# Optimization experiments

Hardware: AMD Instinct MI355X
Metric: run time of the kernel (lower is better)

Reference implementation:

```python
import jax, jax.numpy as jnp
import numpy as np

D = 1024      # d_model
H = 16        # nhead
DH = D // H   # d_head = 64
DC = D // 4   # d_compress = 256
HID = 2048    # dim_feedforward (SwiGLU hidden)
G = 2         # num_groups
EPG = 4       # experts_per_gp
E = G * EPG   # num_experts = 8
TOPK = 2
EPS = 1e-6
B, T = 2, 2048


def _rope_sincos(t, dh):
    inv_freq = 1.0 / (10000.0 ** (jnp.arange(0, dh, 2, dtype=jnp.float32) / dh))
    ang = jnp.arange(t, dtype=jnp.float32)[:, None] * inv_freq[None, :]  # [T, dh/2]
    return jnp.sin(ang), jnp.cos(ang)


def _apply_rope(x, sin, cos):
    # x: [B, H, T, DH]; sin/cos: [T, DH/2] broadcast over B,H
    x1 = x[..., ::2]
    x2 = x[..., 1::2]
    r = jnp.stack([x1 * cos - x2 * sin, x1 * sin + x2 * cos], axis=-1)
    return r.reshape(x.shape)


def _swiglu(x):
    a, b = jnp.split(x, 2, axis=-1)
    return jax.nn.silu(a) * b


def _rmsnorm(x, w):
    return x * jax.lax.rsqrt(jnp.mean(x * x, axis=-1, keepdims=True) + EPS) * w


def reference(src, Wq, Wk_c, Wv_c, Wk, Wv, Wo,
              W_shared_in, W_shared_out, W1_shared, W2_experts,
              Wg_gate, We_gate, group_bias, expert_bias, norm1_w, norm2_w):
    Bb, Tt, C = src.shape
    # ---- Latent attention (K/V compressed to d_c then re-expanded) ----
    q = (src @ Wq).reshape(Bb, Tt, H, DH).transpose(0, 2, 1, 3)
    k = ((src @ Wk_c) @ Wk).reshape(Bb, Tt, H, DH).transpose(0, 2, 1, 3)
    v = ((src @ Wv_c) @ Wv).reshape(Bb, Tt, H, DH).transpose(0, 2, 1, 3)
    sin, cos = _rope_sincos(Tt, DH)
    q = _apply_rope(q, sin, cos)
    k = _apply_rope(k, sin, cos)
    attn = jnp.einsum('bhqd,bhkd->bhqk', q, k) / np.sqrt(DH).astype(np.float32)
    attn = jax.nn.softmax(attn, axis=-1)
    sa = jnp.einsum('bhqk,bhkd->bhqd', attn, v)
    sa = sa.transpose(0, 2, 1, 3).reshape(Bb, Tt, C) @ Wo
    x = _rmsnorm(src + sa, norm1_w)

    # ---- Hierarchical MoE FFN ----
    S = Bb * Tt
    flat = x.reshape(S, C)
    shared = _swiglu(flat @ W_shared_in) @ W_shared_out          # [S, C]
    g_probs = jax.nn.softmax(flat @ Wg_gate + group_bias, -1)    # [S, G]
    g_idx = jnp.argmax(g_probs, axis=-1)                          # [S]
    e_logits = flat @ We_gate + expert_bias                       # [S, E]
    e_group = jnp.arange(E) // EPG
    in_group = e_group[None, :] == g_idx[:, None]                 # [S, E]
    e_probs = jax.nn.softmax(jnp.where(in_group, e_logits, -jnp.inf), -1)
    g_prob = jnp.take_along_axis(g_probs, g_idx[:, None], axis=1)  # [S, 1]
    p_expert = e_probs * g_prob
    topv, topi = jax.lax.top_k(p_expert, TOPK)                    # [S, K]
    # dense combine weights: zero for non-selected experts (same math as dispatch loop)
    w = jnp.zeros((S, E), flat.dtype).at[jnp.arange(S)[:, None], topi].set(topv)
    h = _swiglu(flat @ W1_shared)                                 # [S, HID] (w1 shared by all experts)
    routed = jnp.zeros_like(shared)
    for e in range(E):  # fixed small expert count
        routed = routed + (h @ W2_experts[e]) * w[:, e:e + 1]
    out = x + (shared + routed).reshape(Bb, Tt, C)
    return _rmsnorm(out, norm2_w)


def setup_inputs() -> dict:
    key = jax.random.key(0)
    ks = jax.random.split(key, 14)
    s = 0.02
    return {
        'src': jax.random.normal(ks[0], (B, T, D), jnp.float32),
        'Wq': jax.random.normal(ks[1], (D, D), jnp.float32) * s,
        'Wk_c': jax.random.normal(ks[2], (D, DC), jnp.float32) * s,
        'Wv_c': jax.random.normal(ks[3], (D, DC), jnp.float32) * s,
        'Wk': jax.random.normal(ks[4], (DC, D), jnp.float32) * s,
        'Wv': jax.random.normal(ks[5], (DC, D), jnp.float32) * s,
        'Wo': jax.random.normal(ks[6], (D, D), jnp.float32) * s,
        'W_shared_in': jax.random.normal(ks[7], (D, 2 * HID), jnp.float32) * s,
        'W_shared_out': jax.random.normal(ks[8], (HID, D), jnp.float32) * s,
        'W1_shared': jax.random.normal(ks[9], (D, 2 * HID), jnp.float32) * s,
        'W2_experts': jax.random.normal(ks[10], (E, HID, D), jnp.float32) * s,
        'Wg_gate': jax.random.normal(ks[11], (D, G), jnp.float32) * s,
        'We_gate': jax.random.normal(ks[12], (D, E), jnp.float32) * s,
        'group_bias': jnp.zeros((G,), jnp.float32),
        'expert_bias': jnp.zeros((E,), jnp.float32),
        'norm1_w': jnp.ones((D,), jnp.float32),
        'norm2_w': jnp.ones((D,), jnp.float32),
    }
```

## Files before the change

kernel.cpp:

```cpp
#include <hip/hip_runtime.h>
#include <math.h>

#define D_    1024
#define H_    16
#define DH_   64
#define DC_   256
#define HID_  2048
#define E_    8
#define B_    2
#define T_    2048
#define S_    4096
#define EPS_  1e-6f
#define QKVW_ 3072

typedef unsigned short u16;
typedef short bf16x8 __attribute__((ext_vector_type(8)));
typedef float f32x4 __attribute__((ext_vector_type(4)));

__device__ __forceinline__ float b2f(u16 u) {
    return __uint_as_float(((unsigned int)u) << 16);
}
__device__ __forceinline__ u16 f2b(float f) {
    unsigned int u = __float_as_uint(f);
    u += 0x7FFF + ((u >> 16) & 1);
    return (u16)(u >> 16);
}
__device__ __forceinline__ void g2l16(const u16* g, u16* l) {
    __builtin_amdgcn_global_load_lds(
        (const __attribute__((address_space(1))) void*)g,
        (__attribute__((address_space(3))) void*)l, 16, 0, 0);
}

__global__ __launch_bounds__(256) void conv_t(const float* __restrict__ in,
                                              u16* __restrict__ out,
                                              int K, int N,
                                              long inZ, long outZ, int perm) {
    in  += (long)blockIdx.z * inZ;
    out += (long)blockIdx.z * outZ;
    __shared__ float t[32][33];
    const int n0 = blockIdx.x * 32, k0 = blockIdx.y * 32;
    int src_n0 = n0;
    if (perm) {
        int t64 = n0 >> 6;
        src_n0 = ((n0 & 63) == 0) ? t64 * 32 : (N / 2 + t64 * 32);
    }
    const int tx = threadIdx.x & 31, ty = threadIdx.x >> 5;
#pragma unroll
    for (int i = 0; i < 4; i++)
        t[ty + 8 * i][tx] = in[(long)(k0 + ty + 8 * i) * N + src_n0 + tx];
    __syncthreads();
#pragma unroll
    for (int i = 0; i < 4; i++)
        out[(long)(n0 + ty + 8 * i) * K + k0 + tx] = f2b(t[tx][ty + 8 * i]);
}

__global__ __launch_bounds__(256) void vt_conv(const u16* __restrict__ qkv,
                                               u16* __restrict__ vt) {
    __shared__ u16 t[32][34];
    const int bh = blockIdx.z;
    const int b = bh >> 4, h = bh & 15;
    const int t0 = blockIdx.x * 32, d0 = blockIdx.y * 32;
    const int tx = threadIdx.x & 31, ty = threadIdx.x >> 5;
#pragma unroll
    for (int i = 0; i < 4; i++)
        t[ty + 8 * i][tx] =
            qkv[((long)b * T_ + t0 + ty + 8 * i) * QKVW_ + 2048 + h * 64 + d0 + tx];
    __syncthreads();
#pragma unroll
    for (int i = 0; i < 4; i++)
        vt[((long)bh * 64 + d0 + ty + 8 * i) * T_ + t0 + tx] = t[tx][ty + 8 * i];
}

__global__ __launch_bounds__(256) void convert_bf16(const float* __restrict__ in,
                                                    u16* __restrict__ out, int n4) {
    int i = blockIdx.x * 256 + threadIdx.x;
    if (i >= n4) return;
    float4 f = ((const float4*)in)[i];
    ushort4 o;
    o.x = f2b(f.x); o.y = f2b(f.y); o.z = f2b(f.z); o.w = f2b(f.w);
    ((ushort4*)out)[i] = o;
}

template<int OUTMODE>
__global__ __launch_bounds__(256) void gemm_bf16(const u16* __restrict__ A,
                                                 const u16* __restrict__ Bt,
                                                 void* __restrict__ Cp,
                                                 int N, int K, int ldo,
                                                 void* __restrict__ Cp2) {
    __shared__ u16 As[128 * 32];
    __shared__ u16 Bs[128 * 32];
    const int tid  = threadIdx.x;
    const int lane = tid & 63;
    const int wv   = tid >> 6;
    const int wm   = wv >> 1, wn = wv & 1;
    const long row0 = (long)blockIdx.y * 128;
    const long col0 = (long)blockIdx.x * 128;
    const int Klocal = K / gridDim.z;
    const long koff  = (long)blockIdx.z * Klocal;

    f32x4 acc[4][4];
#pragma unroll
    for (int i = 0; i < 4; i++)
#pragma unroll
        for (int j = 0; j < 4; j++) acc[i][j] = (f32x4){0.f, 0.f, 0.f, 0.f};

    const int sr = tid >> 2;
    const int sc = (tid & 3) << 3;
    const u16* Ag  = A  + (row0 + sr) * (long)K + koff + sc;
    const u16* Ag2 = Ag + 64 * (long)K;
    const u16* Bg  = Bt + (col0 + sr) * (long)K + koff + sc;
    const u16* Bg2 = Bg + 64 * (long)K;
    u16* lA  = As + tid * 8;
    u16* lA2 = As + 2048 + tid * 8;
    u16* lB  = Bs + tid * 8;
    u16* lB2 = Bs + 2048 + tid * 8;

    const int fl = lane & 15;
    const int fk = (lane >> 4) << 3;
    const u16* ArA = As + (wm * 64 + fl) * 32 + fk;
    const u16* BrB = Bs + (wn * 64 + fl) * 32 + fk;

    for (int k0 = 0; k0 < Klocal; k0 += 32) {
        __syncthreads();
        g2l16(Ag + k0, lA);
        g2l16(Ag2 + k0, lA2);
        g2l16(Bg + k0, lB);
        g2l16(Bg2 + k0, lB2);
        __syncthreads();
        bf16x8 af[4], bfr[4];
#pragma unroll
        for (int mi = 0; mi < 4; mi++) af[mi]  = *(const bf16x8*)(ArA + mi * 512);
#pragma unroll
        for (int ni = 0; ni < 4; ni++) bfr[ni] = *(const bf16x8*)(BrB + ni * 512);
#pragma unroll
        for (int mi = 0; mi < 4; mi++)
#pragma unroll
            for (int ni = 0; ni < 4; ni++)
                acc[mi][ni] = __builtin_amdgcn_mfma_f32_16x16x32_bf16(
                    af[mi], bfr[ni], acc[mi][ni], 0, 0, 0);
    }

    const int cr = (lane >> 4) << 2;
    const int cc = lane & 15;
#pragma unroll
    for (int mi = 0; mi < 4; mi++) {
#pragma unroll
        for (int r = 0; r < 4; r++) {
            long grow = row0 + wm * 64 + mi * 16 + cr + r;
#pragma unroll
            for (int ni = 0; ni < 4; ni++) {
                long gcol = col0 + wn * 64 + ni * 16 + cc;
                float v = acc[mi][ni][r];
                if (OUTMODE == 1)      ((u16*)Cp)[grow * ldo + gcol] = f2b(v);
                else if (OUTMODE == 2) ((u16*)Cp)[gcol * ldo + grow] = f2b(v);
                else {
                    float* basep = (float*)(blockIdx.z ? Cp2 : Cp);
                    basep[grow * ldo + gcol] = v;
                }
            }
        }
    }
}

template<int OUTMODE>
__global__ __launch_bounds__(512) void gemm256(const u16* __restrict__ A,
                                               const u16* __restrict__ Bt,
                                               void* __restrict__ Cp,
                                               int K, int ldo) {
    __shared__ u16 As[2][256 * 64];
    __shared__ u16 Bs[2][256 * 64];
    const int tid  = threadIdx.x;
    const int lane = tid & 63;
    const int w    = tid >> 6;
    const int wr   = w >> 2, wc = w & 3;
    const long row0 = (long)blockIdx.y * 256;
    const long col0 = (long)blockIdx.x * 256;

    f32x4 acc[8][4];
#pragma unroll
    for (int i = 0; i < 8; i++)
#pragma unroll
        for (int j = 0; j < 4; j++) acc[i][j] = (f32x4){0.f, 0.f, 0.f, 0.f};

    const int srow = tid >> 3;
    const int sgS  = ((tid & 7) ^ (srow & 7)) << 3;
    const u16* Ag = A  + (row0 + srow) * (long)K + sgS;
    const u16* Bg = Bt + (col0 + srow) * (long)K + sgS;

    const int fl = lane & 15;
    const int fq = lane >> 4;
    const int aoff = (wr * 128 + fl) * 64;
    const int boff = (wc * 64 + fl) * 64;

#define STAGE256(j, buf) do {                                             \
        const long ko_ = (long)(j) * 64;                                  \
        u16* la_ = As[buf] + tid * 8;                                     \
        u16* lb_ = Bs[buf] + tid * 8;                                     \
        _Pragma("unroll")                                                 \
        for (int rr_ = 0; rr_ < 4; rr_++)                                 \
            g2l16(Ag + (long)rr_ * 64 * K + ko_, la_ + rr_ * 4096);       \
        _Pragma("unroll")                                                 \
        for (int rr_ = 0; rr_ < 4; rr_++)                                 \
            g2l16(Bg + (long)rr_ * 64 * K + ko_, lb_ + rr_ * 4096);       \
    } while (0)

    STAGE256(0, 0);
    __syncthreads();
    const int NT = K >> 6;
    for (int j = 0; j < NT; j++) {
        const int buf = j & 1;
        if (j + 1 < NT) STAGE256(j + 1, buf ^ 1);
        const u16* ab = As[buf];
        const u16* bb = Bs[buf];
#pragma unroll
        for (int ks = 0; ks < 2; ks++) {
            const int sw = ((ks * 4 + fq) ^ (fl & 7)) << 3;
            bf16x8 af[8], bfr[4];
#pragma unroll
            for (int mi = 0; mi < 8; mi++)
                af[mi] = *(const bf16x8*)(ab + aoff + mi * 1024 + sw);
#pragma unroll
            for (int ni = 0; ni < 4; ni++)
                bfr[ni] = *(const bf16x8*)(bb + boff + ni * 1024 + sw);
#pragma unroll
            for (int mi = 0; mi < 8; mi++)
#pragma unroll
                for (int ni = 0; ni < 4; ni++)
                    acc[mi][ni] = __builtin_amdgcn_mfma_f32_16x16x32_bf16(
                        af[mi], bfr[ni], acc[mi][ni], 0, 0, 0);
        }
        __syncthreads();
    }

    const int cr = fq << 2;
    const int cc = fl;
#pragma unroll
    for (int mi = 0; mi < 8; mi++) {
#pragma unroll
        for (int r = 0; r < 4; r++) {
            long grow = row0 + wr * 128 + mi * 16 + cr + r;
            if (OUTMODE == 3) {
                u16* outb = (u16*)Cp + (long)(blockIdx.x >> 4) * S_ * HID_;
                u16* hrow = outb + grow * ldo + (blockIdx.x & 15) * 128 + wc * 32;
#pragma unroll
                for (int ni = 0; ni < 2; ni++) {
                    float a = acc[mi][ni][r], b = acc[mi][ni + 2][r];
                    float sig = 1.f / (1.f + __expf(-a));
                    hrow[ni * 16 + cc] = f2b(a * sig * b);
                }
            } else {
#pragma unroll
                for (int ni = 0; ni < 4; ni++) {
                    long gcol = col0 + wc * 64 + ni * 16 + cc;
                    ((u16*)Cp)[grow * ldo + gcol] = f2b(acc[mi][ni][r]);
                }
            }
        }
    }
#undef STAGE256
}

__global__ __launch_bounds__(256) void gemm128p(const u16* __restrict__ A,
                                                const u16* __restrict__ Bt,
                                                float* __restrict__ Cp,
                                                int K, int ldo,
                                                float* __restrict__ Cp2) {
    __shared__ u16 As[2][128 * 64];
    __shared__ u16 Bs[2][128 * 64];
    const int tid  = threadIdx.x;
    const int lane = tid & 63;
    const int wv   = tid >> 6;
    const int wm   = wv >> 1, wn = wv & 1;
    const long row0 = (long)blockIdx.y * 128;
    const long col0 = (long)blockIdx.x * 128;
    const int Klocal = K / gridDim.z;
    const long koff  = (long)blockIdx.z * Klocal;

    f32x4 acc[4][4];
#pragma unroll
    for (int i = 0; i < 4; i++)
#pragma unroll
        for (int j = 0; j < 4; j++) acc[i][j] = (f32x4){0.f, 0.f, 0.f, 0.f};

    const int srow = tid >> 3;
    const int sgS  = ((tid & 7) ^ (srow & 7)) << 3;
    const u16* Ag = A  + (row0 + srow) * (long)K + koff + sgS;
    const u16* Bg = Bt + (col0 + srow) * (long)K + koff + sgS;

    const int fl = lane & 15;
    const int fq = lane >> 4;
    const int aoff = (wm * 64 + fl) * 64;
    const int boff = (wn * 64 + fl) * 64;

#define STAGE128(j, buf) do {                                             \
        const long ko_ = (long)(j) * 64;                                  \
        u16* la_ = As[buf] + tid * 8;                                     \
        u16* lb_ = Bs[buf] + tid * 8;                                     \
        _Pragma("unroll")                                                 \
        for (int rr_ = 0; rr_ < 4; rr_++)                                 \
            g2l16(Ag + (long)rr_ * 32 * K + ko_, la_ + rr_ * 2048);       \
        _Pragma("unroll")                                                 \
        for (int rr_ = 0; rr_ < 4; rr_++)                                 \
            g2l16(Bg + (long)rr_ * 32 * K + ko_, lb_ + rr_ * 2048);       \
    } while (0)

    STAGE128(0, 0);
    __syncthreads();
    const int NT = Klocal >> 6;
    for (int j = 0; j < NT; j++) {
        const int buf = j & 1;
        if (j + 1 < NT) STAGE128(j + 1, buf ^ 1);
        const u16* ab = As[buf];
        const u16* bb = Bs[buf];
#pragma unroll
        for (int ks = 0; ks < 2; ks++) {
            const int sw = ((ks * 4 + fq) ^ (fl & 7)) << 3;
            bf16x8 af[4], bfr[4];
#pragma unroll
            for (int mi = 0; mi < 4; mi++)
                af[mi] = *(const bf16x8*)(ab + aoff + mi * 1024 + sw);
#pragma unroll
            for (int ni = 0; ni < 4; ni++)
                bfr[ni] = *(const bf16x8*)(bb + boff + ni * 1024 + sw);
#pragma unroll
            for (int mi = 0; mi < 4; mi++)
#pragma unroll
                for (int ni = 0; ni < 4; ni++)
                    acc[mi][ni] = __builtin_amdgcn_mfma_f32_16x16x32_bf16(
                        af[mi], bfr[ni], acc[mi][ni], 0, 0, 0);
        }
        __syncthreads();
    }

    float* basep = blockIdx.z ? Cp2 : Cp;
    const int cr = fq << 2;
#pragma unroll
    for (int mi = 0; mi < 4; mi++) {
#pragma unroll
        for (int r = 0; r < 4; r++) {
            long grow = row0 + wm * 64 + mi * 16 + cr + r;
#pragma unroll
            for (int ni = 0; ni < 4; ni++) {
                long gcol = col0 + wn * 64 + ni * 16 + fl;
                basep[grow * ldo + gcol] = acc[mi][ni][r];
            }
        }
    }
#undef STAGE128
}

__global__ __launch_bounds__(256) void routed_gemm(const u16* __restrict__ Hh,
                                                   const u16* __restrict__ W2T,
                                                   const int* __restrict__ list,
                                                   const float* __restrict__ wlist,
                                                   const int* __restrict__ bases,
                                                   const int* __restrict__ counts,
                                                   float* __restrict__ Cout) {
    const int e    = blockIdx.y >> 5;
    const int tile = blockIdx.y & 31;
    const int cnt  = counts[e];
    if (tile * 128 >= cnt) return;
    const int base = bases[e];

    __shared__ u16 As[2][128 * 64];
    __shared__ u16 Bs[2][128 * 64];
    __shared__ int   toks[128];
    __shared__ float wrow[128];

    const int tid = threadIdx.x;
    if (tid < 128) {
        int ridx = tile * 128 + tid;
        if (ridx < cnt) { toks[tid] = list[base + ridx]; wrow[tid] = wlist[base + ridx]; }
        else            { toks[tid] = -1;                wrow[tid] = 0.f; }
    }
    __syncthreads();

    const int lane = tid & 63;
    const int wv   = tid >> 6;
    const int wm   = wv >> 1, wn = wv & 1;
    const long col0 = (long)blockIdx.x * 128;

    f32x4 acc[4][4];
#pragma unroll
    for (int i = 0; i < 4; i++)
#pragma unroll
        for (int j = 0; j < 4; j++) acc[i][j] = (f32x4){0.f, 0.f, 0.f, 0.f};

    const int srow = tid >> 3;
    const int sgS  = ((tid & 7) ^ (srow & 7)) << 3;
    const u16* Apt[4];
#pragma unroll
    for (int rr = 0; rr < 4; rr++) {
        int t = toks[srow + 32 * rr];
        Apt[rr] = Hh + (long)(t < 0 ? 0 : t) * HID_ + sgS;
    }
    const u16* Bg = W2T + (long)e * D_ * HID_ + (col0 + srow) * (long)HID_ + sgS;

    const int fl = lane & 15;
    const int fq = lane >> 4;
    const int aoff = (wm * 64 + fl) * 64;
    const int boff = (wn * 64 + fl) * 64;

#define STAGER(j, buf) do {                                               \
        const long ko_ = (long)(j) * 64;                                  \
        u16* la_ = As[buf] + tid * 8;                                     \
        u16* lb_ = Bs[buf] + tid * 8;                                     \
        _Pragma("unroll")                                                 \
        for (int rr_ = 0; rr_ < 4; rr_++)                                 \
            g2l16(Apt[rr_] + ko_, la_ + rr_ * 2048);                      \
        _Pragma("unroll")                                                 \
        for (int rr_ = 0; rr_ < 4; rr_++)                                 \
            g2l16(Bg + (long)rr_ * 32 * HID_ + ko_, lb_ + rr_ * 2048);    \
    } while (0)

    STAGER(0, 0);
    __syncthreads();
    const int NT = HID_ >> 6;
    for (int j = 0; j < NT; j++) {
        const int buf = j & 1;
        if (j + 1 < NT) STAGER(j + 1, buf ^ 1);
        const u16* ab = As[buf];
        const u16* bb = Bs[buf];
#pragma unroll
        for (int ks = 0; ks < 2; ks++) {
            const int sw = ((ks * 4 + fq) ^ (fl & 7)) << 3;
            bf16x8 af[4], bfr[4];
#pragma unroll
            for (int mi = 0; mi < 4; mi++)
                af[mi] = *(const bf16x8*)(ab + aoff + mi * 1024 + sw);
#pragma unroll
            for (int ni = 0; ni < 4; ni++)
                bfr[ni] = *(const bf16x8*)(bb + boff + ni * 1024 + sw);
#pragma unroll
            for (int mi = 0; mi < 4; mi++)
#pragma unroll
                for (int ni = 0; ni < 4; ni++)
                    acc[mi][ni] = __builtin_amdgcn_mfma_f32_16x16x32_bf16(
                        af[mi], bfr[ni], acc[mi][ni], 0, 0, 0);
        }
        __syncthreads();
    }

    const int cr = fq << 2;
    const int cc = fl;
#pragma unroll
    for (int mi = 0; mi < 4; mi++) {
#pragma unroll
        for (int r = 0; r < 4; r++) {
            int rr = wm * 64 + mi * 16 + cr + r;
            int tk = toks[rr];
            if (tk < 0) continue;
            float wvw = wrow[rr];
            float* crow = Cout + (long)tk * D_ + col0 + wn * 64;
#pragma unroll
            for (int ni = 0; ni < 4; ni++)
                atomicAdd(crow + ni * 16 + cc, acc[mi][ni][r] * wvw);
        }
    }
#undef STAGER
}

__global__ __launch_bounds__(256) void rope_table(float2* __restrict__ tab) {
    int idx = blockIdx.x * 256 + threadIdx.x;
    int t = idx >> 5, i = idx & 31;
    float ang = (float)t * powf(10000.f, -(float)i / 32.f);
    float sn, cs;
    sincosf(ang, &sn, &cs);
    tab[idx] = make_float2(sn, cs);
}

__global__ __launch_bounds__(256) void rope_apply(u16* __restrict__ qkv,
                                                  const float2* __restrict__ tab) {
    long p = (long)blockIdx.x * 256 + threadIdx.x;
    int s  = (int)(p >> 8);
    int c8 = (int)(p & 255) << 3;
    int t  = s & (T_ - 1);
    const float2* tp = tab + t * 32 + ((c8 & 63) >> 1);
    u16* px = qkv + (long)s * QKVW_ + c8;
    bf16x8 v = *(const bf16x8*)px;
    bf16x8 o;
#pragma unroll
    for (int j = 0; j < 4; j++) {
        float x1 = b2f((u16)v[2 * j]), x2 = b2f((u16)v[2 * j + 1]);
        float2 sc = tp[j];
        o[2 * j]     = (short)f2b(x1 * sc.y - x2 * sc.x);
        o[2 * j + 1] = (short)f2b(x1 * sc.x + x2 * sc.y);
    }
    *(bf16x8*)px = o;
}

__global__ __launch_bounds__(512) void attn_kernel(const u16* __restrict__ qkv,
                                                   const u16* __restrict__ vtg,
                                                   u16* __restrict__ sab) {
    __shared__ u16 Ks[128 * 64];
    __shared__ u16 Vs[64 * 128];
    __shared__ u16 Ps[8][16 * 128];
    const int tid  = threadIdx.x;
    const int lane = tid & 63;
    const int w    = tid >> 6;
    const int flat = blockIdx.x + (blockIdx.y << 4);
    const int virt = ((flat & 7) << 6) | (flat >> 3);
    const int qt = virt & 15;
    const int bh = virt >> 4;
    const int b  = bh >> 4, h = bh & 15;
    const long tok0 = (long)b * T_ + qt * 128;
    const int fl = lane & 15;
    const int fq = lane >> 4;

    bf16x8 qf0, qf1;
    {
        const u16* qp = qkv + (tok0 + w * 16 + fl) * QKVW_ + h * 64 + fq * 8;
        qf0 = *(const bf16x8*)qp;
        qf1 = *(const bf16x8*)(qp + 32);
    }

    const u16* kb0 = qkv + ((long)b * T_) * QKVW_ + 1024 + h * 64;
    const u16* vb0 = vtg + ((long)bh * 64) * T_;

    const int kr0 = tid >> 3,         kgg = tid & 7;
    const int kr1 = (tid + 512) >> 3;
    const int vr0 = tid >> 4,         vgg = tid & 15;
    const int vr1 = (tid + 512) >> 4;
    const u16* kp0 = kb0 + (long)kr0 * QKVW_ + ((kgg ^ (kr0 & 7)) << 3);
    const u16* kp1 = kb0 + (long)kr1 * QKVW_ + ((kgg ^ (kr1 & 7)) << 3);
    const u16* vp0 = vb0 + (long)vr0 * T_ + ((vgg ^ (vr0 & 15)) << 3);
    const u16* vp1 = vb0 + (long)vr1 * T_ + ((vgg ^ (vr1 & 15)) << 3);
    u16* kl0 = Ks + tid * 8;
    u16* kl1 = Ks + (tid + 512) * 8;
    u16* vl0 = Vs + tid * 8;
    u16* vl1 = Vs + (tid + 512) * 8;

    bf16x8 kreg0, kreg1, vreg0, vreg1;
    auto stage_load = [&](int kt) {
        const long ko = (long)kt * 128 * QKVW_;
        const int  vo = kt * 128;
        kreg0 = *(const bf16x8*)(kp0 + ko);
        kreg1 = *(const bf16x8*)(kp1 + ko);
        vreg0 = *(const bf16x8*)(vp0 + vo);
        vreg1 = *(const bf16x8*)(vp1 + vo);
    };
    auto stage_write = [&]() {
        *(bf16x8*)kl0 = kreg0;
        *(bf16x8*)kl1 = kreg1;
        *(bf16x8*)vl0 = vreg0;
        *(bf16x8*)vl1 = vreg1;
    };

    float m_[4], l_[4];
    f32x4 oacc[4];
#pragma unroll
    for (int i = 0; i < 4; i++) {
        m_[i] = -1e30f; l_[i] = 0.f;
        oacc[i] = (f32x4){0.f, 0.f, 0.f, 0.f};
    }

    stage_load(0);
    stage_write();
    __syncthreads();

    for (int kt = 0; kt < T_ / 128; kt++) {
        const bool pf = (kt + 1 < T_ / 128);
        if (pf) stage_load(kt + 1);

        f32x4 sacc[8];
#pragma unroll
        for (int ni = 0; ni < 8; ni++) sacc[ni] = (f32x4){0.f, 0.f, 0.f, 0.f};
        __builtin_amdgcn_s_setprio(1);
#pragma unroll
        for (int ks = 0; ks < 2; ks++) {
            bf16x8 qq = ks ? qf1 : qf0;
#pragma unroll
            for (int ni = 0; ni < 8; ni++) {
                bf16x8 kf = *(const bf16x8*)(Ks + (ni * 16 + fl) * 64 +
                                             (((ks * 4 + fq) ^ (fl & 7)) << 3));
                sacc[ni] = __builtin_amdgcn_mfma_f32_16x16x32_bf16(qq, kf, sacc[ni], 0, 0, 0);
            }
        }
        __builtin_amdgcn_s_setprio(0);

        float rmax[4];
#pragma unroll
        for (int r = 0; r < 4; r++) {
            float mm = sacc[0][r];
#pragma unroll
            for (int ni = 1; ni < 8; ni++) mm = fmaxf(mm, sacc[ni][r]);
            rmax[r] = mm * 0.125f;
        }
#pragma unroll
        for (int off = 1; off < 16; off <<= 1)
#pragma unroll
            for (int r = 0; r < 4; r++) rmax[r] = fmaxf(rmax[r], __shfl_xor(rmax[r], off));

        bool grow = false;
        float nm[4];
#pragma unroll
        for (int r = 0; r < 4; r++) {
            nm[r] = fmaxf(m_[r], rmax[r]);
            grow = grow || (rmax[r] > m_[r] + 8.f);
        }
        if (__any(grow)) {
#pragma unroll
            for (int r = 0; r < 4; r++) {
                float a = __expf(m_[r] - nm[r]);
                m_[r] = nm[r];
                l_[r] *= a;
#pragma unroll
                for (int ni = 0; ni < 4; ni++) oacc[ni][r] *= a;
            }
        }

        float psum[4];
#pragma unroll
        for (int r = 0; r < 4; r++) psum[r] = 0.f;
        u16* pst = Ps[w];
#pragma unroll
        for (int ni = 0; ni < 8; ni++) {
            int colg = ni * 2 + (fl >> 3);
            int cl   = fl & 7;
#pragma unroll
            for (int r = 0; r < 4; r++) {
                int row = fq * 4 + r;
                float p = __expf(sacc[ni][r] * 0.125f - m_[r]);
                psum[r] += p;
                pst[row * 128 + ((colg ^ (row & 15)) << 3) + cl] = f2b(p);
            }
        }
#pragma unroll
        for (int off = 1; off < 16; off <<= 1)
#pragma unroll
            for (int r = 0; r < 4; r++) psum[r] += __shfl_xor(psum[r], off);
#pragma unroll
        for (int r = 0; r < 4; r++) l_[r] += psum[r];

        __builtin_amdgcn_s_setprio(1);
#pragma unroll
        for (int ks = 0; ks < 4; ks++) {
            bf16x8 pfr = *(const bf16x8*)(pst + fl * 128 +
                                          (((ks * 4 + fq) ^ fl) << 3));
#pragma unroll
            for (int ni = 0; ni < 4; ni++) {
                bf16x8 vf = *(const bf16x8*)(Vs + (ni * 16 + fl) * 128 +
                                             (((ks * 4 + fq) ^ fl) << 3));
                oacc[ni] = __builtin_amdgcn_mfma_f32_16x16x32_bf16(pfr, vf, oacc[ni], 0, 0, 0);
            }
        }
        __builtin_amdgcn_s_setprio(0);

        __syncthreads();
        if (pf) {
            stage_write();
            __syncthreads();
        }
    }

#pragma unroll
    for (int r = 0; r < 4; r++) {
        float inv = 1.f / l_[r];
        u16* op = sab + (tok0 + w * 16 + fq * 4 + r) * D_ + h * 64 + fl;
#pragma unroll
        for (int ni = 0; ni < 4; ni++) op[ni * 16] = f2b(oacc[ni][r] * inv);
    }
}

template<int BF>
__global__ __launch_bounds__(256) void rmsnorm_res(const float* __restrict__ a,
                                                   const float* __restrict__ b,
                                                   const float* __restrict__ b2,
                                                   const float* __restrict__ w,
                                                   float* __restrict__ outf,
                                                   u16* __restrict__ outb) {
    const int s = blockIdx.x;
    const float* ar = a + (long)s * D_;
    const float* br = b + (long)s * D_;
    const float* cr2 = b2 + (long)s * D_;
    float y[4];
    float ss = 0.f;
#pragma unroll
    for (int kx = 0; kx < 4; kx++) {
        int j = threadIdx.x + kx * 256;
        y[kx] = ar[j] + br[j] + cr2[j];
        ss += y[kx] * y[kx];
    }
    __shared__ float red[4];
#pragma unroll
    for (int off = 32; off > 0; off >>= 1) ss += __shfl_down(ss, off);
    int lane = threadIdx.x & 63, wv = threadIdx.x >> 6;
    if (lane == 0) red[wv] = ss;
    __syncthreads();
    float tot = red[0] + red[1] + red[2] + red[3];
    float scl = rsqrtf(tot / (float)D_ + EPS_);
    float* orow = outf + (long)s * D_;
#pragma unroll
    for (int kx = 0; kx < 4; kx++) {
        int j = threadIdx.x + kx * 256;
        float v = y[kx] * scl * w[j];
        orow[j] = v;
        if (BF) outb[(long)s * D_ + j] = f2b(v);
    }
}

__global__ __launch_bounds__(256) void gate_kernel(const float* __restrict__ x,
                                                   const float* __restrict__ Wg,
                                                   const float* __restrict__ We,
                                                   const float* __restrict__ gb,
                                                   const float* __restrict__ eb,
                                                   int* __restrict__ tok_e,
                                                   float* __restrict__ tok_w) {
    const int wave = threadIdx.x >> 6;
    const int lane = threadIdx.x & 63;
    const int s = blockIdx.x * 4 + wave;
    const float* xr = x + (long)s * D_;
    float g0 = 0.f, g1 = 0.f;
    float ee[8];
#pragma unroll
    for (int e = 0; e < 8; e++) ee[e] = 0.f;
    for (int j = lane; j < D_; j += 64) {
        float xv = xr[j];
        g0 += xv * Wg[j * 2 + 0];
        g1 += xv * Wg[j * 2 + 1];
#pragma unroll
        for (int e = 0; e < 8; e++) ee[e] += xv * We[j * 8 + e];
    }
#pragma unroll
    for (int off = 32; off > 0; off >>= 1) {
        g0 += __shfl_down(g0, off);
        g1 += __shfl_down(g1, off);
#pragma unroll
        for (int e = 0; e < 8; e++) ee[e] += __shfl_down(ee[e], off);
    }
    if (lane == 0) {
        g0 += gb[0];
        g1 += gb[1];
        int gidx = (g1 > g0) ? 1 : 0;
        float gm = fmaxf(g0, g1);
        float p0 = expf(g0 - gm), p1 = expf(g1 - gm);
        float gprob = (gidx ? p1 : p0) / (p0 + p1);
        int base = gidx * 4;
        float pe[4];
        float em = -1e30f;
#pragma unroll
        for (int i = 0; i < 4; i++) {
            pe[i] = ee[base + i] + eb[base + i];
            em = fmaxf(em, pe[i]);
        }
        float sum = 0.f;
#pragma unroll
        for (int i = 0; i < 4; i++) { pe[i] = expf(pe[i] - em); sum += pe[i]; }
        float inv = gprob / sum;
#pragma unroll
        for (int i = 0; i < 4; i++) pe[i] *= inv;
        int i1 = 0;
        for (int i = 1; i < 4; i++) if (pe[i] > pe[i1]) i1 = i;
        int i2 = -1;
        for (int i = 0; i < 4; i++) {
            if (i == i1) continue;
            if (i2 < 0 || pe[i] > pe[i2]) i2 = i;
        }
        tok_e[s * 2 + 0] = base + i1;
        tok_e[s * 2 + 1] = base + i2;
        tok_w[s * 2 + 0] = pe[i1];
        tok_w[s * 2 + 1] = pe[i2];
    }
}

__global__ __launch_bounds__(256) void route_build(const int* __restrict__ tok_e,
                                                   const float* __restrict__ tok_w,
                                                   int* __restrict__ counts_g,
                                                   int* __restrict__ bases_g,
                                                   int* __restrict__ list,
                                                   float* __restrict__ wlist) {
    __shared__ int cnt[E_], bas[E_], cur[E_];
    const int tid = threadIdx.x;
    if (tid < E_) cnt[tid] = 0;
    __syncthreads();
    for (int i = tid; i < 2 * S_; i += 256) atomicAdd(&cnt[tok_e[i]], 1);
    __syncthreads();
    if (tid == 0) {
        int acc = 0;
        for (int e = 0; e < E_; e++) { bas[e] = acc; cur[e] = acc; acc += cnt[e]; }
    }
    __syncthreads();
    if (tid < E_) { counts_g[tid] = cnt[tid]; bases_g[tid] = bas[tid]; }
    for (int i = tid; i < 2 * S_; i += 256) {
        int e = tok_e[i];
        int p = atomicAdd(&cur[e], 1);
        list[p] = i >> 1;
        wlist[p] = tok_w[i];
    }
}

extern "C" void kernel_launch(void* const* d_in, const int* in_sizes, int n_in,
                              void* d_out, int out_size, void* d_ws, size_t ws_size,
                              hipStream_t stream) {
    const float* src  = (const float*)d_in[0];
    const float* Wq   = (const float*)d_in[1];
    const float* Wk_c = (const float*)d_in[2];
    const float* Wv_c = (const float*)d_in[3];
    const float* Wk   = (const float*)d_in[4];
    const float* Wv   = (const float*)d_in[5];
    const float* Wo   = (const float*)d_in[6];
    const float* Wsin = (const float*)d_in[7];
    const float* Wsout= (const float*)d_in[8];
    const float* W1   = (const float*)d_in[9];
    const float* W2   = (const float*)d_in[10];
    const float* Wg   = (const float*)d_in[11];
    const float* We   = (const float*)d_in[12];
    const float* gb   = (const float*)d_in[13];
    const float* eb   = (const float*)d_in[14];
    const float* n1w  = (const float*)d_in[15];
    const float* n2w  = (const float*)d_in[16];
    float* out = (float*)d_out;

    const size_t MB = 1u << 20;
    char* w8 = (char*)d_ws;
    u16*  qkv   = (u16*)(w8);
    u16*  vtg   = (u16*)(w8 + 24 * MB);
    float* oproj0 = (float*)(w8);
    float* oproj1 = (float*)(w8 + 16 * MB);
    u16*  w2t   = (u16*)(w8);
    u16*  WkcB  = (u16*)(w8 + 24 * MB);
    u16*  WvcB  = (u16*)(w8 + 24 * MB + 512 * 1024);
    u16*  WkTs  = (u16*)(w8 + 25 * MB);
    u16*  WvTs  = (u16*)(w8 + 25 * MB + 512 * 1024);
    u16*  sab   = (u16*)(w8 + 32 * MB);
    float* tokw = (float*)(w8 + 32 * MB);
    float* wlist = tokw + 2 * S_;
    int* toke   = (int*)(wlist + 2 * S_);
    int* list   = toke + 2 * S_;
    int* counts = list + 2 * S_;
    int* bases  = counts + E_;
    float* x1   = (float*)(w8 + 40 * MB);
    float* ffn0 = (float*)(w8 + 56 * MB);
    u16*  x1b   = (u16*)(w8 + 72 * MB);
    u16*  hbuf  = (u16*)(w8 + 80 * MB);
    u16*  srcb  = (u16*)(w8 + 96 * MB);
    float2* rtab= (float2*)(w8 + 104 * MB);
    u16*  hbuf2 = (u16*)(w8 + 96 * MB);
    u16*  WqkvT = (u16*)(w8 + 112 * MB);
    u16*  WsoutT= (u16*)(w8 + 112 * MB);
    u16*  WoT   = (u16*)(w8 + 118 * MB);
    u16*  WsinT = (u16*)(w8 + 120 * MB);
    u16*  W1T   = (u16*)(w8 + 128 * MB);
    float* ffn1 = (float*)(w8 + 120 * MB);

    dim3 blk(256);

    conv_t<<<dim3(32, 32), blk, 0, stream>>>(Wq, WqkvT, 1024, 1024, 0, 0, 0);
    convert_bf16<<<dim3(D_ * DC_ / 4 / 256), blk, 0, stream>>>(Wk_c, WkcB, D_ * DC_ / 4);
    convert_bf16<<<dim3(D_ * DC_ / 4 / 256), blk, 0, stream>>>(Wv_c, WvcB, D_ * DC_ / 4);
    conv_t<<<dim3(32, 8), blk, 0, stream>>>(Wk, WkTs, 256, 1024, 0, 0, 0);
    conv_t<<<dim3(32, 8), blk, 0, stream>>>(Wv, WvTs, 256, 1024, 0, 0, 0);
    gemm_bf16<2><<<dim3(8, 8), blk, 0, stream>>>(WkcB, WkTs, WqkvT + 1024 * 1024, 1024, 256, 1024, nullptr);
    gemm_bf16<2><<<dim3(8, 8), blk, 0, stream>>>(WvcB, WvTs, WqkvT + 2048 * 1024, 1024, 256, 1024, nullptr);

    convert_bf16<<<dim3(S_ * D_ / 4 / 256), blk, 0, stream>>>(src, srcb, S_ * D_ / 4);

    gemm256<1><<<dim3(QKVW_ / 256, S_ / 256), dim3(512), 0, stream>>>(srcb, WqkvT, qkv, 1024, QKVW_);

    conv_t<<<dim3(32, 32), blk, 0, stream>>>(Wo, WoT, 1024, 1024, 0, 0, 0);
    conv_t<<<dim3(128, 32), blk, 0, stream>>>(Wsin, WsinT, 1024, 4096, 0, 0, 1);
    conv_t<<<dim3(32, 64), blk, 0, stream>>>(Wsout, WsoutT, 2048, 1024, 0, 0, 0);
    conv_t<<<dim3(128, 32), blk, 0, stream>>>(W1, W1T, 1024, 4096, 0, 0, 1);

    rope_table<<<dim3(T_ * 32 / 256), blk, 0, stream>>>(rtab);
    rope_apply<<<dim3(S_ * 2048 / 8 / 256), blk, 0, stream>>>(qkv, rtab);

    vt_conv<<<dim3(T_ / 32, 2, B_ * H_), blk, 0, stream>>>(qkv, vtg);
    attn_kernel<<<dim3(T_ / 128, B_ * H_), dim3(512), 0, stream>>>(qkv, vtg, sab);

    gemm128p<<<dim3(8, 32, 2), blk, 0, stream>>>(sab, WoT, oproj0, 1024, 1024, oproj1);
    rmsnorm_res<1><<<dim3(S_), blk, 0, stream>>>(src, oproj0, oproj1, n1w, x1, x1b);

    gemm256<3><<<dim3(8192 / 256, S_ / 256), dim3(512), 0, stream>>>(x1b, WsinT, hbuf, 1024, 2048);

    gemm128p<<<dim3(8, 32, 2), blk, 0, stream>>>(hbuf, WsoutT, ffn0, 2048, 1024, ffn1);

    gate_kernel<<<dim3(S_ / 4), blk, 0, stream>>>(x1, Wg, We, gb, eb, toke, tokw);
    route_build<<<dim3(1), blk, 0, stream>>>(toke, tokw, counts, bases, list, wlist);

    conv_t<<<dim3(32, 64, 8), blk, 0, stream>>>(W2, w2t, 2048, 1024,
                                                (long)HID_ * D_, (long)D_ * HID_, 0);
    routed_gemm<<<dim3(8, E_ * 32), blk, 0, stream>>>(hbuf2, w2t, list, wlist,
                                                      bases, counts, ffn0);

    rmsnorm_res<0><<<dim3(S_), blk, 0, stream>>>(x1, ffn0, ffn1, n2w, out, (u16*)nullptr);
}
```

Baseline: 657.9 us.

## Split routed expert GEMM over K and simplify to single-buffered 32-wide tiles

The routed expert GEMM now splits the hidden (K) dimension across a new grid z dimension of 2, with each block accumulating its partial result into the output through the existing atomicAdd epilogue. This doubles the number of blocks so that sparsely populated expert tiles fill more of the GPU. The inner loop is also rewritten with K-step 32, no double buffering and no LDS swizzle. That shrinks shared memory use but adds two barriers per step, exposes load latency and may cause LDS bank conflicts.

```diff
diff --git a/kernel.cpp b/kernel.cpp
--- a/kernel.cpp
+++ b/kernel.cpp
@@ -362,8 +362,8 @@
     if (tile * 128 >= cnt) return;
     const int base = bases[e];
 
-    __shared__ u16 As[2][128 * 64];
-    __shared__ u16 Bs[2][128 * 64];
+    __shared__ u16 As[128 * 32];
+    __shared__ u16 Bs[128 * 32];
     __shared__ int   toks[128];
     __shared__ float wrow[128];
 
@@ -379,6 +379,8 @@
     const int wv   = tid >> 6;
     const int wm   = wv >> 1, wn = wv & 1;
     const long col0 = (long)blockIdx.x * 128;
+    const int Klocal = HID_ / gridDim.z;
+    const long koff  = (long)blockIdx.z * Klocal;
 
     f32x4 acc[4][4];
 #pragma unroll
@@ -386,63 +388,45 @@
 #pragma unroll
         for (int j = 0; j < 4; j++) acc[i][j] = (f32x4){0.f, 0.f, 0.f, 0.f};
 
-    const int srow = tid >> 3;
-    const int sgS  = ((tid & 7) ^ (srow & 7)) << 3;
-    const u16* Apt[4];
-#pragma unroll
-    for (int rr = 0; rr < 4; rr++) {
-        int t = toks[srow + 32 * rr];
-        Apt[rr] = Hh + (long)(t < 0 ? 0 : t) * HID_ + sgS;
-    }
-    const u16* Bg = W2T + (long)e * D_ * HID_ + (col0 + srow) * (long)HID_ + sgS;
+    const int sr = tid >> 2;
+    const int sc = (tid & 3) << 3;
+    const int t1 = toks[sr], t2 = toks[sr + 64];
+    const u16* Ag  = Hh + (long)(t1 < 0 ? 0 : t1) * HID_ + koff + sc;
+    const u16* Ag2 = Hh + (long)(t2 < 0 ? 0 : t2) * HID_ + koff + sc;
+    const u16* Bg  = W2T + (long)e * D_ * HID_ + (col0 + sr) * (long)HID_ + koff + sc;
+    const u16* Bg2 = Bg + 64 * (long)HID_;
+    u16* lA  = As + tid * 8;
+    u16* lA2 = As + 2048 + tid * 8;
+    u16* lB  = Bs + tid * 8;
+    u16* lB2 = Bs + 2048 + tid * 8;
 
     const int fl = lane & 15;
-    const int fq = lane >> 4;
-    const int aoff = (wm * 64 + fl) * 64;
-    const int boff = (wn * 64 + fl) * 64;
-
-#define STAGER(j, buf) do {                                               \
-        const long ko_ = (long)(j) * 64;                                  \
-        u16* la_ = As[buf] + tid * 8;                                     \
-        u16* lb_ = Bs[buf] + tid * 8;                                     \
-        _Pragma("unroll")                                                 \
-        for (int rr_ = 0; rr_ < 4; rr_++)                                 \
-            g2l16(Apt[rr_] + ko_, la_ + rr_ * 2048);                      \
-        _Pragma("unroll")                                                 \
-        for (int rr_ = 0; rr_ < 4; rr_++)                                 \
-            g2l16(Bg + (long)rr_ * 32 * HID_ + ko_, lb_ + rr_ * 2048);    \
-    } while (0)
-
-    STAGER(0, 0);
-    __syncthreads();
-    const int NT = HID_ >> 6;
-    for (int j = 0; j < NT; j++) {
-        const int buf = j & 1;
-        if (j + 1 < NT) STAGER(j + 1, buf ^ 1);
-        const u16* ab = As[buf];
-        const u16* bb = Bs[buf];
-#pragma unroll
-        for (int ks = 0; ks < 2; ks++) {
-            const int sw = ((ks * 4 + fq) ^ (fl & 7)) << 3;
-            bf16x8 af[4], bfr[4];
-#pragma unroll
-            for (int mi = 0; mi < 4; mi++)
-                af[mi] = *(const bf16x8*)(ab + aoff + mi * 1024 + sw);
+    const int fk = (lane >> 4) << 3;
+    const u16* ArA = As + (wm * 64 + fl) * 32 + fk;
+    const u16* BrB = Bs + (wn * 64 + fl) * 32 + fk;
+
+    for (int k0 = 0; k0 < Klocal; k0 += 32) {
+        __syncthreads();
+        g2l16(Ag + k0, lA);
+        g2l16(Ag2 + k0, lA2);
+        g2l16(Bg + k0, lB);
+        g2l16(Bg2 + k0, lB2);
+        __syncthreads();
+        bf16x8 af[4], bfr[4];
+#pragma unroll
+        for (int mi = 0; mi < 4; mi++) af[mi]  = *(const bf16x8*)(ArA + mi * 512);
+#pragma unroll
+        for (int ni = 0; ni < 4; ni++) bfr[ni] = *(const bf16x8*)(BrB + ni * 512);
+#pragma unroll
+        for (int mi = 0; mi < 4; mi++)
 #pragma unroll
             for (int ni = 0; ni < 4; ni++)
-                bfr[ni] = *(const bf16x8*)(bb + boff + ni * 1024 + sw);
-#pragma unroll
-            for (int mi = 0; mi < 4; mi++)
-#pragma unroll
-                for (int ni = 0; ni < 4; ni++)
-                    acc[mi][ni] = __builtin_amdgcn_mfma_f32_16x16x32_bf16(
-                        af[mi], bfr[ni], acc[mi][ni], 0, 0, 0);
-        }
-        __syncthreads();
-    }
-
-    const int cr = fq << 2;
-    const int cc = fl;
+                acc[mi][ni] = __builtin_amdgcn_mfma_f32_16x16x32_bf16(
+                    af[mi], bfr[ni], acc[mi][ni], 0, 0, 0);
+    }
+
+    const int cr = (lane >> 4) << 2;
+    const int cc = lane & 15;
 #pragma unroll
     for (int mi = 0; mi < 4; mi++) {
 #pragma unroll
@@ -457,7 +441,6 @@
                 atomicAdd(crow + ni * 16 + cc, acc[mi][ni][r] * wvw);
         }
     }
-#undef STAGER
 }
 
 __global__ __launch_bounds__(256) void rope_table(float2* __restrict__ tab) {
@@ -880,8 +863,8 @@
 
     conv_t<<<dim3(32, 64, 8), blk, 0, stream>>>(W2, w2t, 2048, 1024,
                                                 (long)HID_ * D_, (long)D_ * HID_, 0);
-    routed_gemm<<<dim3(8, E_ * 32), blk, 0, stream>>>(hbuf2, w2t, list, wlist,
-                                                      bases, counts, ffn0);
+    routed_gemm<<<dim3(8, E_ * 32, 2), blk, 0, stream>>>(hbuf2, w2t, list, wlist,
+                                                         bases, counts, ffn0);
 
     rmsnorm_res<0><<<dim3(S_), blk, 0, stream>>>(x1, ffn0, ffn1, n2w, out, (u16*)nullptr);
 }
```

Result: no change. 649.4 us (-1.3%).
